# Performance work log

Hardware: AMD Instinct MI355X
Metric: run time of the kernel (lower is better)

The kernel has to match this reference:

```python
import jax, jax.numpy as jnp
import numpy as np

NUM_EXPERT = 16
IN_DIM = 1024
OUT_DIM = 3072
TOTAL_TOKENS = 16384  # tokens pre-grouped by expert, contiguous blocks


def setup_inputs() -> dict:
    key = jax.random.key(0)
    k1, k2, k3 = jax.random.split(key, 3)
    inp = jax.random.normal(k1, (TOTAL_TOKENS, IN_DIM), dtype=jnp.float32)
    # per-expert token counts (sum == TOTAL_TOKENS); even split here
    fwd_expert_count = jnp.full((NUM_EXPERT,), TOTAL_TOKENS // NUM_EXPERT, dtype=jnp.int64)
    scale = 1.0 / np.sqrt(IN_DIM)
    weight = jax.random.normal(k2, (NUM_EXPERT, OUT_DIM, IN_DIM), dtype=jnp.float32) * scale
    bias = jax.random.normal(k3, (NUM_EXPERT, OUT_DIM), dtype=jnp.float32) * scale
    return {"inp": inp, "fwd_expert_count": fwd_expert_count, "weight": weight, "bias": bias}


def reference(inp, fwd_expert_count, weight, bias):
    # Grouped GEMM: token block e (size fwd_expert_count[e]) uses expert e's
    # weight: y = x @ W_e^T + b_e.  Tokens are contiguous per expert, so
    # expert id per token = repeat(arange(E), counts).
    T = inp.shape[0]
    E = weight.shape[0]
    expert_id = jnp.repeat(jnp.arange(E), fwd_expert_count, total_repeat_length=T)  # [T]
    out = jnp.zeros((T, weight.shape[1]), dtype=inp.dtype)
    # small fixed structural loop over experts (E=16); each iter is a dense GEMM
    for e in range(E):
        ye = inp @ weight[e].T + bias[e]  # [T, out_dim]
        out = jnp.where((expert_id == e)[:, None], ye, out)
    return out
```

## Files before the change

kernel.cpp:

```cpp
#include <hip/hip_runtime.h>

typedef __attribute__((ext_vector_type(8)))  _Float16 f16x8;
typedef __attribute__((ext_vector_type(2)))  __fp16   fp16x2;
typedef __attribute__((ext_vector_type(4)))  float    f32x4;

#define TT 16384
#define KD 1024
#define ND 3072
#define NE 16
#define ASZ (TT * KD)
#define WSZ (NE * ND * KD)
#define NEED_WS ((size_t)(ASZ + WSZ) * 2)

#define BM 256
#define BN 256
#define BK 64
#define NSTEP (KD / BK)
#define ROWB (BK * 2)

#define BAR() __builtin_amdgcn_s_barrier()
#define WAIT_VM(n) asm volatile("s_waitcnt vmcnt(" #n ")" ::: "memory")

__device__ __forceinline__ int swz(int row, int kbyte) {
    return row * ROWB + (kbyte ^ ((row & 7) << 4));
}

__device__ __forceinline__ int find_expert(const void* cntp, int row0) {
    const int* w = (const int*)cntp;
    int oddsum = 0;
    #pragma unroll
    for (int i = 1; i < 16; i += 2) oddsum |= w[i];
    int e = 0;
    long long cum = 0;
    if (oddsum == 0) {
        const long long* c = (const long long*)cntp;
        #pragma unroll
        for (int i = 0; i < NE; ++i) { if ((long long)row0 >= cum) e = i; cum += c[i]; }
    } else {
        #pragma unroll
        for (int i = 0; i < NE; ++i) { if ((long long)row0 >= cum) e = i; cum += w[i]; }
    }
    return e;
}

__device__ __forceinline__ void gl16(const void* g, void* l) {
    __builtin_amdgcn_global_load_lds(
        (const __attribute__((address_space(1))) unsigned int*)g,
        (__attribute__((address_space(3))) unsigned int*)l, 16, 0, 0);
}

__global__ __launch_bounds__(256) void cvt_kernel(const float* __restrict__ A,
                                                  const float* __restrict__ W,
                                                  _Float16* __restrict__ dst) {
    size_t i = ((size_t)blockIdx.x * 256 + threadIdx.x) * 8;
    const float* src = (i < (size_t)ASZ) ? (A + i) : (W + (i - ASZ));
    f32x4 v0 = *(const f32x4*)src;
    f32x4 v1 = *(const f32x4*)(src + 4);
    f16x8 h;
    h[0] = (_Float16)v0[0]; h[1] = (_Float16)v0[1];
    h[2] = (_Float16)v0[2]; h[3] = (_Float16)v0[3];
    h[4] = (_Float16)v1[0]; h[5] = (_Float16)v1[1];
    h[6] = (_Float16)v1[2]; h[7] = (_Float16)v1[3];
    *(f16x8*)(dst + i) = h;
}

#define MFMA16(AF, BF, MH, NH) do {                                          \
    __builtin_amdgcn_s_setprio(1);                                           \
    _Pragma("unroll")                                                        \
    for (int kk = 0; kk < 2; ++kk)                                           \
        _Pragma("unroll")                                                    \
        for (int m = 0; m < 4; ++m)                                          \
            _Pragma("unroll")                                                \
            for (int n = 0; n < 2; ++n)                                      \
                acc[MH][NH][m][n] = __builtin_amdgcn_mfma_f32_16x16x32_f16(  \
                    AF[kk][m], BF[kk][n], acc[MH][NH][m][n], 0, 0, 0);       \
    __builtin_amdgcn_s_setprio(0);                                           \
} while (0)

__launch_bounds__(512, 2)
__global__ void gemm16(const _Float16* __restrict__ A16,
                       const void* __restrict__ cnt,
                       const _Float16* __restrict__ W16,
                       const float* __restrict__ bias,
                       float* __restrict__ Y) {
    __shared__ __align__(16) char Aslot[2][2][128 * ROWB];
    __shared__ __align__(16) char Bslot[2][2][128 * ROWB];

    const int nwg = gridDim.x;
    const int bid0 = blockIdx.x;
    const int wgid = (bid0 & 7) * (nwg >> 3) + (bid0 >> 3);

    const int mt = wgid / (ND / BN);
    const int nt = wgid % (ND / BN);
    const int row0 = mt * BM;
    const int col0 = nt * BN;

    const int e = find_expert(cnt, row0);
    const _Float16* We = W16 + (size_t)e * ND * KD;

    const int tid = threadIdx.x;
    const int l = tid & 63;
    const int w = tid >> 6;
    const int wr = w >> 2;
    const int wc = w & 3;
    const int lr = l & 15;
    const int lk = l >> 4;

    const int laneoff = ((l & 7) * 16) ^ ((l >> 3) << 4);
    const size_t srcoff = (size_t)(w * 16 + (l >> 3)) * (KD * 2) + laneoff;

    const char* gA0 = (const char*)A16 + (size_t)row0 * (KD * 2);
    const char* gA1 = gA0 + (size_t)128 * (KD * 2);
    const char* gB0 = (const char*)We + (size_t)col0 * (KD * 2);
    const char* gB1 = gB0 + (size_t)128 * (KD * 2);

    auto stage_half = [&](const char* ghalf, char* slot, int t) {
        const char* s = ghalf + t * 128 + srcoff;
        gl16(s,                slot + w * 2048);
        gl16(s + 8 * (KD * 2), slot + w * 2048 + 1024);
    };

    f32x4 acc[2][2][4][2] = {};
    f16x8 af0[2][4], af1[2][4], bf0[2][2], bf1[2][2];

    auto read_A = [&](f16x8 (&af)[2][4], const char* slot) {
        #pragma unroll
        for (int kk = 0; kk < 2; ++kk)
            #pragma unroll
            for (int m = 0; m < 4; ++m) {
                int r = wr * 64 + m * 16 + lr;
                af[kk][m] = *(const f16x8*)&slot[swz(r, kk * 64 + lk * 16)];
            }
    };
    auto read_B = [&](f16x8 (&bf)[2][2], const char* slot) {
        #pragma unroll
        for (int kk = 0; kk < 2; ++kk)
            #pragma unroll
            for (int n = 0; n < 2; ++n) {
                int r = wc * 32 + n * 16 + lr;
                bf[kk][n] = *(const f16x8*)&slot[swz(r, kk * 64 + lk * 16)];
            }
    };

    stage_half(gA0, &Aslot[0][0][0], 0);
    stage_half(gB0, &Bslot[0][0][0], 0);
    stage_half(gA1, &Aslot[1][0][0], 0);
    stage_half(gB1, &Bslot[1][0][0], 0);

    for (int t = 0; t < NSTEP - 1; ++t) {
        const int par = t & 1, nxt = par ^ 1;
        WAIT_VM(4);
        BAR();
        read_A(af0, Aslot[0][par]);
        read_B(bf0, Bslot[0][par]);
        stage_half(gA0, &Aslot[0][nxt][0], t + 1);
        MFMA16(af0, bf0, 0, 0);
        WAIT_VM(4);
        BAR();
        read_A(af1, Aslot[1][par]);
        stage_half(gB0, &Bslot[0][nxt][0], t + 1);
        MFMA16(af1, bf0, 1, 0);
        WAIT_VM(4);
        BAR();
        read_B(bf1, Bslot[1][par]);
        stage_half(gA1, &Aslot[1][nxt][0], t + 1);
        MFMA16(af1, bf1, 1, 1);
        stage_half(gB1, &Bslot[1][nxt][0], t + 1);
        MFMA16(af0, bf1, 0, 1);
    }
    {
        const int par = (NSTEP - 1) & 1;
        WAIT_VM(4);
        BAR();
        read_A(af0, Aslot[0][par]);
        read_B(bf0, Bslot[0][par]);
        MFMA16(af0, bf0, 0, 0);
        WAIT_VM(2);
        BAR();
        read_A(af1, Aslot[1][par]);
        MFMA16(af1, bf0, 1, 0);
        WAIT_VM(0);
        BAR();
        read_B(bf1, Bslot[1][par]);
        MFMA16(af1, bf1, 1, 1);
        MFMA16(af0, bf1, 0, 1);
    }

    float bv[2][2];
    #pragma unroll
    for (int nh = 0; nh < 2; ++nh)
        #pragma unroll
        for (int n = 0; n < 2; ++n)
            bv[nh][n] = bias[(size_t)e * ND + col0 + nh * 128 + wc * 32 + n * 16 + lr];
    #pragma unroll
    for (int mh = 0; mh < 2; ++mh)
        #pragma unroll
        for (int nh = 0; nh < 2; ++nh)
            #pragma unroll
            for (int m = 0; m < 4; ++m)
                #pragma unroll
                for (int j = 0; j < 4; ++j) {
                    int r = row0 + mh * 128 + wr * 64 + m * 16 + lk * 4 + j;
                    float* yp = Y + (size_t)r * ND + col0 + nh * 128 + wc * 32 + lr;
                    yp[0]  = acc[mh][nh][m][0][j] + bv[nh][0];
                    yp[16] = acc[mh][nh][m][1][j] + bv[nh][1];
                }
}

__launch_bounds__(512, 2)
__global__ void fallback_gemm(const float* __restrict__ A,
                              const void* __restrict__ cnt,
                              const float* __restrict__ W,
                              const float* __restrict__ bias,
                              float* __restrict__ Y) {
    __shared__ __align__(16) char ldsbuf[2][2][BM * ROWB];

    const int nwg = gridDim.x;
    const int bid0 = blockIdx.x;
    const int wgid = (bid0 & 7) * (nwg >> 3) + (bid0 >> 3);

    const int mt = wgid / (ND / BN);
    const int nt = wgid % (ND / BN);
    const int row0 = mt * BM;
    const int col0 = nt * BN;

    const int e = find_expert(cnt, row0);
    const float* We = W + (size_t)e * ND * KD;

    const int tid = threadIdx.x;
    const int lane = tid & 63;
    const int w = tid >> 6;
    const int wr = w >> 2;
    const int wc = w & 3;
    const int lr = lane & 15;
    const int lk = lane >> 4;

    int soff[4];
    size_t aoff[4], boff[4];
    #pragma unroll
    for (int c = 0; c < 4; ++c) {
        int q = c * 512 + tid;
        int r = q >> 3;
        int kb = (q & 7) * 8;
        soff[c] = swz(r, kb * 2);
        aoff[c] = (size_t)(row0 + r) * KD + kb;
        boff[c] = (size_t)(col0 + r) * KD + kb;
    }

    f32x4 ra[4][2], rb[4][2];

    auto load_regs = [&](int ks) {
        const int k0 = ks * BK;
        #pragma unroll
        for (int c = 0; c < 4; ++c) {
            const float* ap = A + aoff[c] + k0;
            ra[c][0] = *(const f32x4*)ap;
            ra[c][1] = *(const f32x4*)(ap + 4);
            const float* bp = We + boff[c] + k0;
            rb[c][0] = *(const f32x4*)bp;
            rb[c][1] = *(const f32x4*)(bp + 4);
        }
    };

    auto write_lds = [&](int buf) {
        #pragma unroll
        for (int c = 0; c < 4; ++c) {
            union { f16x8 v; fp16x2 h[4]; } ua, ub;
            ua.h[0] = __builtin_amdgcn_cvt_pkrtz(ra[c][0][0], ra[c][0][1]);
            ua.h[1] = __builtin_amdgcn_cvt_pkrtz(ra[c][0][2], ra[c][0][3]);
            ua.h[2] = __builtin_amdgcn_cvt_pkrtz(ra[c][1][0], ra[c][1][1]);
            ua.h[3] = __builtin_amdgcn_cvt_pkrtz(ra[c][1][2], ra[c][1][3]);
            ub.h[0] = __builtin_amdgcn_cvt_pkrtz(rb[c][0][0], rb[c][0][1]);
            ub.h[1] = __builtin_amdgcn_cvt_pkrtz(rb[c][0][2], rb[c][0][3]);
            ub.h[2] = __builtin_amdgcn_cvt_pkrtz(rb[c][1][0], rb[c][1][1]);
            ub.h[3] = __builtin_amdgcn_cvt_pkrtz(rb[c][1][2], rb[c][1][3]);
            *(f16x8*)&ldsbuf[buf][0][soff[c]] = ua.v;
            *(f16x8*)&ldsbuf[buf][1][soff[c]] = ub.v;
        }
    };

    f32x4 acc[8][4] = {};

    auto compute = [&](const char* Asb, const char* Bsb) {
        #pragma unroll
        for (int kk = 0; kk < 2; ++kk) {
            f16x8 af[8], bf[4];
            #pragma unroll
            for (int m = 0; m < 8; ++m) {
                int r = wr * 128 + m * 16 + lr;
                af[m] = *(const f16x8*)&Asb[swz(r, kk * 64 + lk * 16)];
            }
            #pragma unroll
            for (int n = 0; n < 4; ++n) {
                int r = wc * 64 + n * 16 + lr;
                bf[n] = *(const f16x8*)&Bsb[swz(r, kk * 64 + lk * 16)];
            }
            #pragma unroll
            for (int m = 0; m < 8; ++m)
                #pragma unroll
                for (int n = 0; n < 4; ++n)
                    acc[m][n] = __builtin_amdgcn_mfma_f32_16x16x32_f16(
                        af[m], bf[n], acc[m][n], 0, 0, 0);
        }
    };

    load_regs(0);
    write_lds(0);
    __syncthreads();

    for (int t = 0; t < NSTEP; ++t) {
        const int buf = t & 1;
        if (t + 1 < NSTEP) load_regs(t + 1);
        compute(ldsbuf[buf][0], ldsbuf[buf][1]);
        __syncthreads();
        if (t + 1 < NSTEP) write_lds(buf ^ 1);
        __syncthreads();
    }

    const int cb = col0 + wc * 64;
    const int rb0_ = row0 + wr * 128;
    float bv[4];
    #pragma unroll
    for (int n = 0; n < 4; ++n) bv[n] = bias[(size_t)e * ND + cb + n * 16 + lr];
    #pragma unroll
    for (int m = 0; m < 8; ++m) {
        #pragma unroll
        for (int j = 0; j < 4; ++j) {
            int r = rb0_ + m * 16 + lk * 4 + j;
            float* yp = Y + (size_t)r * ND + cb + lr;
            #pragma unroll
            for (int n = 0; n < 4; ++n)
                yp[n * 16] = acc[m][n][j] + bv[n];
        }
    }
}

extern "C" void kernel_launch(void* const* d_in, const int* in_sizes, int n_in,
                              void* d_out, int out_size, void* d_ws, size_t ws_size,
                              hipStream_t stream) {
    const float* inp  = (const float*)d_in[0];
    const void*  cnt  = d_in[1];
    const float* wgt  = (const float*)d_in[2];
    const float* bias = (const float*)d_in[3];
    float* out = (float*)d_out;

    dim3 grid((TT / BM) * (ND / BN));
    dim3 block(512);

    if (ws_size >= NEED_WS) {
        _Float16* ws16 = (_Float16*)d_ws;
        cvt_kernel<<<dim3((ASZ + WSZ) / (8 * 256)), dim3(256), 0, stream>>>(inp, wgt, ws16);
        gemm16<<<grid, block, 0, stream>>>(ws16, cnt, ws16 + ASZ, bias, out);
    } else {
        fallback_gemm<<<grid, block, 0, stream>>>(inp, cnt, wgt, bias, out);
    }
}
```

Baseline: 197.0 us.

## Fuse activation fp32-to-fp16 conversion into GEMM A-tile staging

```diff
diff --git a/kernel.cpp b/kernel.cpp
--- a/kernel.cpp
+++ b/kernel.cpp
@@ -1,6 +1,7 @@
 #include <hip/hip_runtime.h>
 
 typedef __attribute__((ext_vector_type(8)))  _Float16 f16x8;
+typedef __attribute__((ext_vector_type(4)))  _Float16 f16x4;
 typedef __attribute__((ext_vector_type(2)))  __fp16   fp16x2;
 typedef __attribute__((ext_vector_type(4)))  float    f32x4;
 
@@ -8,9 +9,8 @@
 #define KD 1024
 #define ND 3072
 #define NE 16
-#define ASZ (TT * KD)
 #define WSZ (NE * ND * KD)
-#define NEED_WS ((size_t)(ASZ + WSZ) * 2)
+#define NEED_WS ((size_t)WSZ * 2)
 
 #define BM 256
 #define BN 256
@@ -19,6 +19,10 @@
 #define ROWB (BK * 2)
 
 #define BAR() __builtin_amdgcn_s_barrier()
+#define LGKM0_BAR() do {                                        \
+    asm volatile("s_waitcnt lgkmcnt(0)" ::: "memory");          \
+    __builtin_amdgcn_s_barrier();                               \
+} while (0)
 #define WAIT_VM(n) asm volatile("s_waitcnt vmcnt(" #n ")" ::: "memory")
 
 __device__ __forceinline__ int swz(int row, int kbyte) {
@@ -49,13 +53,12 @@
         (__attribute__((address_space(3))) unsigned int*)l, 16, 0, 0);
 }
 
-__global__ __launch_bounds__(256) void cvt_kernel(const float* __restrict__ A,
-                                                  const float* __restrict__ W,
-                                                  _Float16* __restrict__ dst) {
+__global__ __launch_bounds__(256) void cvt_w(const float* __restrict__ W,
+                                             _Float16* __restrict__ dst) {
     size_t i = ((size_t)blockIdx.x * 256 + threadIdx.x) * 8;
-    const float* src = (i < (size_t)ASZ) ? (A + i) : (W + (i - ASZ));
-    f32x4 v0 = *(const f32x4*)src;
-    f32x4 v1 = *(const f32x4*)(src + 4);
+    const float* src = W + i;
+    f32x4 v0 = __builtin_nontemporal_load((const f32x4*)src);
+    f32x4 v1 = __builtin_nontemporal_load((const f32x4*)(src + 4));
     f16x8 h;
     h[0] = (_Float16)v0[0]; h[1] = (_Float16)v0[1];
     h[2] = (_Float16)v0[2]; h[3] = (_Float16)v0[3];
@@ -78,7 +81,7 @@
 } while (0)
 
 __launch_bounds__(512, 2)
-__global__ void gemm16(const _Float16* __restrict__ A16,
+__global__ void gemm16(const float* __restrict__ A,
                        const void* __restrict__ cnt,
                        const _Float16* __restrict__ W16,
                        const float* __restrict__ bias,
@@ -107,23 +110,48 @@
     const int lk = l >> 4;
 
     const int laneoff = ((l & 7) * 16) ^ ((l >> 3) << 4);
-    const size_t srcoff = (size_t)(w * 16 + (l >> 3)) * (KD * 2) + laneoff;
-
-    const char* gA0 = (const char*)A16 + (size_t)row0 * (KD * 2);
-    const char* gA1 = gA0 + (size_t)128 * (KD * 2);
+    const size_t bsrcoff = (size_t)(w * 16 + (l >> 3)) * (KD * 2) + laneoff;
     const char* gB0 = (const char*)We + (size_t)col0 * (KD * 2);
     const char* gB1 = gB0 + (size_t)128 * (KD * 2);
 
-    auto stage_half = [&](const char* ghalf, char* slot, int t) {
-        const char* s = ghalf + t * 128 + srcoff;
+    auto stageB = [&](const char* ghalf, char* slot, int t) {
+        const char* s = ghalf + t * 128 + bsrcoff;
         gl16(s,                slot + w * 2048);
         gl16(s + 8 * (KD * 2), slot + w * 2048 + 1024);
     };
 
+    int aoffA[4], aswz[4];
+    #pragma unroll
+    for (int c = 0; c < 4; ++c) {
+        int q = c * 512 + tid;
+        int r = q >> 4;
+        int qd = q & 15;
+        aoffA[c] = r * KD + qd * 4;
+        aswz[c]  = swz(r, qd * 8);
+    }
+    const float* gA0f = A + (size_t)row0 * KD;
+    const float* gA1f = gA0f + (size_t)128 * KD;
+
+    f32x4 rA0[4], rA1[4];
+    auto issueA = [&](f32x4 (&rA)[4], const float* ghalf, int t) {
+        const float* s = ghalf + t * 64;
+        #pragma unroll
+        for (int c = 0; c < 4; ++c) rA[c] = *(const f32x4*)(s + aoffA[c]);
+    };
+    auto writeA = [&](const f32x4 (&rA)[4], char* slot) {
+        #pragma unroll
+        for (int c = 0; c < 4; ++c) {
+            union { f16x4 v; fp16x2 h[2]; } u;
+            u.h[0] = __builtin_amdgcn_cvt_pkrtz(rA[c][0], rA[c][1]);
+            u.h[1] = __builtin_amdgcn_cvt_pkrtz(rA[c][2], rA[c][3]);
+            *(f16x4*)&slot[aswz[c]] = u.v;
+        }
+    };
+
     f32x4 acc[2][2][4][2] = {};
-    f16x8 af0[2][4], af1[2][4], bf0[2][2], bf1[2][2];
-
-    auto read_A = [&](f16x8 (&af)[2][4], const char* slot) {
+    f16x8 af[2][4], bf0[2][2], bf1[2][2];
+
+    auto read_af = [&](const char* slot) {
         #pragma unroll
         for (int kk = 0; kk < 2; ++kk)
             #pragma unroll
@@ -132,7 +160,7 @@
                 af[kk][m] = *(const f16x8*)&slot[swz(r, kk * 64 + lk * 16)];
             }
     };
-    auto read_B = [&](f16x8 (&bf)[2][2], const char* slot) {
+    auto read_bf = [&](f16x8 (&bf)[2][2], const char* slot) {
         #pragma unroll
         for (int kk = 0; kk < 2; ++kk)
             #pragma unroll
@@ -142,48 +170,54 @@
             }
     };
 
-    stage_half(gA0, &Aslot[0][0][0], 0);
-    stage_half(gB0, &Bslot[0][0][0], 0);
-    stage_half(gA1, &Aslot[1][0][0], 0);
-    stage_half(gB1, &Bslot[1][0][0], 0);
+    issueA(rA0, gA0f, 0);
+    stageB(gB0, &Bslot[0][0][0], 0);
+    stageB(gB1, &Bslot[1][0][0], 0);
+    WAIT_VM(4);
+    writeA(rA0, &Aslot[0][0][0]);
+    issueA(rA1, gA1f, 0);
+    WAIT_VM(0);
+    writeA(rA1, &Aslot[1][0][0]);
 
     for (int t = 0; t < NSTEP - 1; ++t) {
         const int par = t & 1, nxt = par ^ 1;
+        LGKM0_BAR();
+        read_af(Aslot[0][par]);
+        read_bf(bf0, Bslot[0][par]);
+        issueA(rA0, gA0f, t + 1);
+        MFMA16(af, bf0, 0, 0);
+        BAR();
         WAIT_VM(4);
+        read_bf(bf1, Bslot[1][par]);
+        stageB(gB0, &Bslot[0][nxt][0], t + 1);
+        MFMA16(af, bf1, 0, 1);
         BAR();
-        read_A(af0, Aslot[0][par]);
-        read_B(bf0, Bslot[0][par]);
-        stage_half(gA0, &Aslot[0][nxt][0], t + 1);
-        MFMA16(af0, bf0, 0, 0);
-        WAIT_VM(4);
-        BAR();
-        read_A(af1, Aslot[1][par]);
-        stage_half(gB0, &Bslot[0][nxt][0], t + 1);
-        MFMA16(af1, bf0, 1, 0);
-        WAIT_VM(4);
-        BAR();
-        read_B(bf1, Bslot[1][par]);
-        stage_half(gA1, &Aslot[1][nxt][0], t + 1);
-        MFMA16(af1, bf1, 1, 1);
-        stage_half(gB1, &Bslot[1][nxt][0], t + 1);
-        MFMA16(af0, bf1, 0, 1);
-    }
+        read_af(Aslot[1][par]);
+        issueA(rA1, gA1f, t + 1);
+        WAIT_VM(6);
+        writeA(rA0, &Aslot[0][nxt][0]);
+        MFMA16(af, bf0, 1, 0);
+        LGKM0_BAR();
+        stageB(gB1, &Bslot[1][nxt][0], t + 1);
+        WAIT_VM(2);
+        writeA(rA1, &Aslot[1][nxt][0]);
+        MFMA16(af, bf1, 1, 1);
+    }
+
     {
         const int par = (NSTEP - 1) & 1;
-        WAIT_VM(4);
+        LGKM0_BAR();
+        read_af(Aslot[0][par]);
+        read_bf(bf0, Bslot[0][par]);
+        MFMA16(af, bf0, 0, 0);
         BAR();
-        read_A(af0, Aslot[0][par]);
-        read_B(bf0, Bslot[0][par]);
-        MFMA16(af0, bf0, 0, 0);
-        WAIT_VM(2);
+        WAIT_VM(0);
+        read_bf(bf1, Bslot[1][par]);
+        MFMA16(af, bf1, 0, 1);
         BAR();
-        read_A(af1, Aslot[1][par]);
-        MFMA16(af1, bf0, 1, 0);
-        WAIT_VM(0);
-        BAR();
-        read_B(bf1, Bslot[1][par]);
-        MFMA16(af1, bf1, 1, 1);
-        MFMA16(af0, bf1, 0, 1);
+        read_af(Aslot[1][par]);
+        MFMA16(af, bf0, 1, 0);
+        MFMA16(af, bf1, 1, 1);
     }
 
     float bv[2][2];
@@ -348,9 +382,9 @@
     dim3 block(512);
 
     if (ws_size >= NEED_WS) {
-        _Float16* ws16 = (_Float16*)d_ws;
-        cvt_kernel<<<dim3((ASZ + WSZ) / (8 * 256)), dim3(256), 0, stream>>>(inp, wgt, ws16);
-        gemm16<<<grid, block, 0, stream>>>(ws16, cnt, ws16 + ASZ, bias, out);
+        _Float16* w16 = (_Float16*)d_ws;
+        cvt_w<<<dim3(WSZ / (8 * 256)), dim3(256), 0, stream>>>(wgt, w16);
+        gemm16<<<grid, block, 0, stream>>>(inp, cnt, w16, bias, out);
     } else {
         fallback_gemm<<<grid, block, 0, stream>>>(inp, cnt, wgt, bias, out);
     }
```

Result: slower. 227.3 us (+15.4%).
